# Kernel tuning notes

Hardware: AMD Instinct MI355X
Metric: run time of the kernel (lower is better)

Reference implementation:

```python
import jax, jax.numpy as jnp
import numpy as np

B, T, D = 2, 1024, 1024
H, HKV = 16, 8
HD = D // H           # 64
NREP = H // HKV       # 2
NLAYERS = 3
MAXKV = T * NLAYERS   # 3072
EPS = 1e-5


def setup_inputs() -> dict:
    key = jax.random.key(0)
    ks = jax.random.split(key, 8)
    # rotary tables over full accumulated-KV range
    inv_freq = 1.0 / (10000.0 ** (jnp.arange(0, HD, 2, dtype=jnp.float32) / HD))  # (HD/2,)
    t = jnp.arange(MAXKV, dtype=jnp.float32)
    freqs = jnp.outer(t, inv_freq)  # (MAXKV, HD/2)
    return {
        "x": jax.random.normal(ks[0], (B, T, D), jnp.float32),
        "cos": jnp.cos(freqs),
        "sin": jnp.sin(freqs),
        "q_w": jax.random.normal(ks[1], (NLAYERS, D, D), jnp.float32) * 0.02,
        "k_w": jax.random.normal(ks[2], (NLAYERS, D // NREP, D), jnp.float32) * 0.02,
        "v_w": jax.random.normal(ks[3], (NLAYERS, D // NREP, D), jnp.float32) * 0.02,
        "ln_w": jnp.ones((NLAYERS, D), jnp.float32),
        "lam": jax.random.normal(ks[4], (NLAYERS,), jnp.float32) * 0.1,
        "out_w": jax.random.normal(ks[5], (D, D), jnp.float32) * 0.02,
        "final_ln_w": jnp.ones((D,), jnp.float32),
        "alpha": jnp.ones((1,), jnp.float32),
    }


def rmsnorm(x, w):
    return x * jax.lax.rsqrt(jnp.mean(x * x, axis=-1, keepdims=True) + EPS) * w


def rope(x, cos, sin):
    # x: (B, L, h, HD); cos/sin: (MAXKV, HD/2); flash_attn non-interleaved rotary
    L = x.shape[1]
    c = jnp.concatenate([cos[:L], cos[:L]], axis=-1)[None, :, None, :]
    s = jnp.concatenate([sin[:L], sin[:L]], axis=-1)[None, :, None, :]
    x1, x2 = jnp.split(x, 2, axis=-1)
    rot = jnp.concatenate([-x2, x1], axis=-1)
    return x * c + rot * s


def reference(x, cos, sin, q_w, k_w, v_w, ln_w, lam, out_w, final_ln_w, alpha):
    scale = HD ** -0.5
    # lambda weights: layernorm over sigmoid of the 3 scalars (biased var, eps=1e-5)
    s = jax.nn.sigmoid(lam)
    lw = (s - s.mean()) * jax.lax.rsqrt(s.var() + EPS)
    qidx = jnp.arange(T)
    k_list, v_list = [], []
    acc = jnp.zeros_like(x)
    for i in range(NLAYERS):
        q = (x @ q_w[i].T).reshape(B, T, H, HD)
        k = (x @ k_w[i].T).reshape(B, T, HKV, HD)
        v = (x @ v_w[i].T).reshape(B, T, HKV, HD)
        k_list.append(k)
        v_list.append(v)
        K = jnp.concatenate(k_list, axis=1)  # (B, L, HKV, HD), L=(i+1)*T
        V = jnp.concatenate(v_list, axis=1)
        L = K.shape[1]
        qr = rope(q, cos, sin)
        Kr = rope(K, cos, sin)  # whole buffer re-rotated each layer, as in original
        Kr = jnp.repeat(Kr, NREP, axis=2)  # GQA expand
        Vr = jnp.repeat(V, NREP, axis=2)
        scores = jnp.einsum('bqhd,bkhd->bhqk', qr, Kr) * scale
        # flash_attn causal=True with kv_len > q_len aligns bottom-right
        mask = jnp.arange(L)[None, :] <= (qidx + (L - T))[:, None]
        scores = jnp.where(mask[None, None], scores, -jnp.inf)
        attn = jax.nn.softmax(scores, axis=-1)
        o = jnp.einsum('bhqk,bkhd->bqhd', attn, Vr).reshape(B, T, D)
        acc = acc + rmsnorm(o, ln_w[i]) * lw[i]
    out = rmsnorm(acc + alpha * x, final_ln_w)
    return out @ out_w.T
```

## Files before the change

### kernel.cpp

```cpp
#include <hip/hip_runtime.h>
#include <type_traits>
#include <utility>

typedef unsigned short u16;
typedef unsigned int u32;
typedef short short8 __attribute__((ext_vector_type(8)));
typedef __bf16 bf16x8 __attribute__((ext_vector_type(8)));
typedef float floatx4 __attribute__((ext_vector_type(4)));

template <typename V, typename = void> struct MfmaTakes : std::false_type {};
template <typename V>
struct MfmaTakes<V, std::void_t<decltype(__builtin_amdgcn_mfma_f32_16x16x32_bf16(
    std::declval<V>(), std::declval<V>(), std::declval<floatx4>(), 0, 0, 0))>>
    : std::true_type {};

template <typename V>
__device__ __forceinline__ floatx4 mfma_impl(V a, V b, floatx4 c, std::true_type) {
  return __builtin_amdgcn_mfma_f32_16x16x32_bf16(a, b, c, 0, 0, 0);
}
template <typename V>
__device__ __forceinline__ floatx4 mfma_impl(V a, V b, floatx4 c, std::false_type) {
  return __builtin_amdgcn_mfma_f32_16x16x32_bf16(
      __builtin_bit_cast(bf16x8, a), __builtin_bit_cast(bf16x8, b), c, 0, 0, 0);
}
__device__ __forceinline__ floatx4 MFMA16(short8 a, short8 b, floatx4 c) {
  return mfma_impl<short8>(a, b, c, MfmaTakes<short8>{});
}

__device__ __forceinline__ u16 f2bf(float f) {
  union { float f; unsigned u; } x; x.f = f;
  unsigned r = (x.u + 0x7fffu + ((x.u >> 16) & 1u)) >> 16;
  return (u16)r;
}
__device__ __forceinline__ float bf2f(u16 v) {
  union { unsigned u; float f; } x; x.u = ((unsigned)v) << 16; return x.f;
}
__device__ __forceinline__ u32 packbf(float lo, float hi) {
  return (__float_as_uint(hi) & 0xffff0000u) | (__float_as_uint(lo) >> 16);
}

#if defined(__has_builtin)
#if __has_builtin(__builtin_amdgcn_global_load_lds)
#define HAS_GLLDS 1
#endif
#endif
__device__ __forceinline__ void stage16(const u16* g, u16* lbase, int lane) {
#ifdef HAS_GLLDS
  __builtin_amdgcn_global_load_lds(
      (__attribute__((address_space(1))) void*)(g),
      (__attribute__((address_space(3))) void*)(lbase), 16, 0, 0);
#else
  *(uint4*)(lbase + lane * 8) = *(const uint4*)g;
#endif
}

__global__ __launch_bounds__(256) void prep_kernel(
    const float* __restrict__ x, const float* __restrict__ qw,
    const float* __restrict__ kw, const float* __restrict__ vw,
    const float* __restrict__ outw, const float* __restrict__ lam,
    u16* __restrict__ xb, u16* __restrict__ wcat, u16* __restrict__ outwb,
    float* __restrict__ lwbuf) {
  size_t gid = (size_t)blockIdx.x * 256 + threadIdx.x;
  if (gid == 0) {
    float s0 = 1.f / (1.f + expf(-lam[0]));
    float s1 = 1.f / (1.f + expf(-lam[1]));
    float s2 = 1.f / (1.f + expf(-lam[2]));
    float mean = (s0 + s1 + s2) * (1.f / 3.f);
    float d0 = s0 - mean, d1 = s1 - mean, d2 = s2 - mean;
    float var = (d0 * d0 + d1 * d1 + d2 * d2) * (1.f / 3.f);
    float r = rsqrtf(var + 1e-5f);
    lwbuf[0] = d0 * r; lwbuf[1] = d1 * r; lwbuf[2] = d2 * r;
  }
  if (gid < 524288) {
    float4 v = ((const float4*)x)[gid];
    ushort4 o; o.x = f2bf(v.x); o.y = f2bf(v.y); o.z = f2bf(v.z); o.w = f2bf(v.w);
    ((ushort4*)xb)[gid] = o;
    return;
  }
  size_t g2 = gid - 524288;
  if (g2 < 1572864) {
    int col4 = (int)(g2 & 255);
    int n = (int)(g2 >> 8);
    int layer = n >> 11, r = n & 2047;
    const float* srcrow;
    if (r < 1024) srcrow = qw + ((size_t)(layer * 1024 + r) << 10);
    else if (r < 1536) srcrow = kw + ((size_t)(layer * 512 + (r - 1024)) << 10);
    else srcrow = vw + ((size_t)(layer * 512 + (r - 1536)) << 10);
    float4 v = ((const float4*)srcrow)[col4];
    ushort4 o; o.x = f2bf(v.x); o.y = f2bf(v.y); o.z = f2bf(v.z); o.w = f2bf(v.w);
    ((ushort4*)wcat)[g2] = o;
    return;
  }
  size_t g3 = g2 - 1572864;
  if (g3 < 262144) {
    float4 v = ((const float4*)outw)[g3];
    ushort4 o; o.x = f2bf(v.x); o.y = f2bf(v.y); o.z = f2bf(v.z); o.w = f2bf(v.w);
    ((ushort4*)outwb)[g3] = o;
  }
}

__global__ __launch_bounds__(256) void gemm128(
    const u16* __restrict__ A, const u16* __restrict__ Bw,
    void* __restrict__ Cp, int N, int K, int obf16) {
  __shared__ u16 As[128][64];
  __shared__ u16 Bs[128][64];
  const unsigned flat = blockIdx.x;
  const int bm = (flat >> 3) & 15;
  const int bn = ((flat >> 7) << 3) + (flat & 7);
  const int tid = threadIdx.x;
  const int wave = tid >> 6, lane = tid & 63;
  const int quad = lane >> 4, l16 = lane & 15;
  const int wm = wave & 1, wn = wave >> 1;
  const int srow = lane >> 3, skc = (lane & 7) * 8;
  floatx4 acc[4][4];
#pragma unroll
  for (int i = 0; i < 4; i++)
#pragma unroll
    for (int j = 0; j < 4; j++) { acc[i][j][0] = 0.f; acc[i][j][1] = 0.f; acc[i][j][2] = 0.f; acc[i][j][3] = 0.f; }
  const u16* Abase = A + (size_t)(bm * 128) * K;
  const u16* Bbase = Bw + (size_t)(bn * 128) * K;
  for (int k0 = 0; k0 < K; k0 += 64) {
    __syncthreads();
#pragma unroll
    for (int i = 0; i < 4; i++) {
      int ch = wave * 4 + i;
      stage16(Abase + (size_t)(ch * 8 + srow) * K + k0 + skc, &As[ch * 8][0], lane);
      stage16(Bbase + (size_t)(ch * 8 + srow) * K + k0 + skc, &Bs[ch * 8][0], lane);
    }
    __syncthreads();
#pragma unroll
    for (int kf = 0; kf < 2; kf++) {
      short8 af[4], bf[4];
#pragma unroll
      for (int mi = 0; mi < 4; mi++)
        af[mi] = *(const short8*)(&As[wm * 64 + mi * 16 + l16][kf * 32 + quad * 8]);
#pragma unroll
      for (int ni = 0; ni < 4; ni++)
        bf[ni] = *(const short8*)(&Bs[wn * 64 + ni * 16 + l16][kf * 32 + quad * 8]);
#pragma unroll
      for (int mi = 0; mi < 4; mi++)
#pragma unroll
        for (int ni = 0; ni < 4; ni++)
          acc[mi][ni] = MFMA16(af[mi], bf[ni], acc[mi][ni]);
    }
  }
  float* Cf = (float*)Cp;
  u16* Cb = (u16*)Cp;
#pragma unroll
  for (int mi = 0; mi < 4; mi++)
#pragma unroll
    for (int ni = 0; ni < 4; ni++)
#pragma unroll
      for (int r = 0; r < 4; r++) {
        int row = bm * 128 + wm * 64 + mi * 16 + quad * 4 + r;
        int col = bn * 128 + wn * 64 + ni * 16 + l16;
        if (obf16) Cb[(size_t)row * N + col] = f2bf(acc[mi][ni][r]);
        else Cf[(size_t)row * N + col] = acc[mi][ni][r];
      }
}

__global__ __launch_bounds__(256) void gemm_bt(
    const u16* __restrict__ A, const u16* __restrict__ Bw,
    float* __restrict__ C, int N, int K) {
  __shared__ u16 As[64][72];
  __shared__ u16 Bs[64][72];
  const int bm = blockIdx.x, bn = blockIdx.y;
  const int tid = threadIdx.x;
  const int wave = tid >> 6, lane = tid & 63;
  const int quad = lane >> 4, l16 = lane & 15;
  const int lr = tid >> 2, lc = (tid & 3) << 4;
  floatx4 acc[4];
#pragma unroll
  for (int i = 0; i < 4; i++) { acc[i][0] = 0.f; acc[i][1] = 0.f; acc[i][2] = 0.f; acc[i][3] = 0.f; }
  const u16* Arow = A + (size_t)(bm * 64 + lr) * K;
  const u16* Brow = Bw + (size_t)(bn * 64 + lr) * K;
  for (int k0 = 0; k0 < K; k0 += 64) {
    __syncthreads();
    *(uint4*)(&As[lr][lc])     = *(const uint4*)(Arow + k0 + lc);
    *(uint4*)(&As[lr][lc + 8]) = *(const uint4*)(Arow + k0 + lc + 8);
    *(uint4*)(&Bs[lr][lc])     = *(const uint4*)(Brow + k0 + lc);
    *(uint4*)(&Bs[lr][lc + 8]) = *(const uint4*)(Brow + k0 + lc + 8);
    __syncthreads();
    const int mrow = wave * 16 + l16;
    short8 a0 = *(const short8*)(&As[mrow][quad * 8]);
    short8 a1 = *(const short8*)(&As[mrow][32 + quad * 8]);
#pragma unroll
    for (int ns = 0; ns < 4; ns++) {
      short8 b0 = *(const short8*)(&Bs[ns * 16 + l16][quad * 8]);
      short8 b1 = *(const short8*)(&Bs[ns * 16 + l16][32 + quad * 8]);
      acc[ns] = MFMA16(a0, b0, acc[ns]);
      acc[ns] = MFMA16(a1, b1, acc[ns]);
    }
  }
#pragma unroll
  for (int ns = 0; ns < 4; ns++)
#pragma unroll
    for (int r = 0; r < 4; r++) {
      int row = bm * 64 + wave * 16 + quad * 4 + r;
      int col = bn * 64 + ns * 16 + l16;
      C[(size_t)row * N + col] = acc[ns][r];
    }
}

__global__ __launch_bounds__(256) void reshape_kernel(
    const u16* __restrict__ qkvb, const float* __restrict__ cosb,
    const float* __restrict__ sinb, u16* __restrict__ qr,
    u16* __restrict__ kr, u16* __restrict__ vtg) {
  __shared__ u16 T[64][72];
  const int bid = blockIdx.x, tid = threadIdx.x;
  union U8 { uint4 v; u16 s[8]; };
  union F8 { float4 v[2]; float f[8]; };
  if (bid < 2304) {
    unsigned gid = (unsigned)bid * 256 + tid;
    if (gid < 393216u) {
      int d8 = gid & 3, t = (gid >> 2) & 1023, h = (gid >> 12) & 15;
      int b = (gid >> 16) & 1, layer = gid >> 17;
      size_t src = (size_t)(b * 1024 + t) * 6144 + layer * 2048 + h * 64 + d8 * 8;
      U8 xa, xc; xa.v = *(const uint4*)(qkvb + src); xc.v = *(const uint4*)(qkvb + src + 32);
      F8 C, S;
      const float4* cp = (const float4*)(cosb + (size_t)t * 32 + d8 * 8);
      const float4* sp = (const float4*)(sinb + (size_t)t * 32 + d8 * 8);
      C.v[0] = cp[0]; C.v[1] = cp[1]; S.v[0] = sp[0]; S.v[1] = sp[1];
      U8 o1, o2;
#pragma unroll
      for (int j = 0; j < 8; j++) {
        float x1 = bf2f(xa.s[j]), x2 = bf2f(xc.s[j]);
        o1.s[j] = f2bf((x1 * C.f[j] - x2 * S.f[j]) * 0.125f);
        o2.s[j] = f2bf((x2 * C.f[j] + x1 * S.f[j]) * 0.125f);
      }
      size_t dst = ((((size_t)layer * 2 + b) * 16 + h) * 1024 + t) * 64 + d8 * 8;
      *(uint4*)(qr + dst) = o1.v;
      *(uint4*)(qr + dst + 32) = o2.v;
      return;
    }
    unsigned g2 = gid - 393216u;
    if (g2 < 196608u) {
      int d8 = g2 & 3, t = (g2 >> 2) & 1023, h = (g2 >> 12) & 7;
      int b = (g2 >> 15) & 1, layer = g2 >> 16;
      int pos = layer * 1024 + t;
      size_t src = (size_t)(b * 1024 + t) * 6144 + layer * 2048 + 1024 + h * 64 + d8 * 8;
      U8 xa, xc; xa.v = *(const uint4*)(qkvb + src); xc.v = *(const uint4*)(qkvb + src + 32);
      F8 C, S;
      const float4* cp = (const float4*)(cosb + (size_t)pos * 32 + d8 * 8);
      const float4* sp = (const float4*)(sinb + (size_t)pos * 32 + d8 * 8);
      C.v[0] = cp[0]; C.v[1] = cp[1]; S.v[0] = sp[0]; S.v[1] = sp[1];
      U8 o1, o2;
#pragma unroll
      for (int j = 0; j < 8; j++) {
        float x1 = bf2f(xa.s[j]), x2 = bf2f(xc.s[j]);
        o1.s[j] = f2bf(x1 * C.f[j] - x2 * S.f[j]);
        o2.s[j] = f2bf(x2 * C.f[j] + x1 * S.f[j]);
      }
      size_t dst = (((size_t)b * 8 + h) * 3072 + pos) * 64 + d8 * 8;
      *(uint4*)(kr + dst) = o1.v;
      *(uint4*)(kr + dst + 32) = o2.v;
    }
    return;
  }
  const int b2 = bid - 2304;
  const int xt = b2 & 15;
  const int y = b2 >> 4;
  const int layer = y >> 4, b = (y >> 3) & 1, h = y & 7;
  const int t0 = xt * 64;
  {
    const int p = tid >> 2, dc = (tid & 3) * 16;
    const u16* src = qkvb + (size_t)(b * 1024 + t0 + p) * 6144 + layer * 2048 + 1536 + h * 64 + dc;
    U8 u0, u1;
    u0.v = *(const uint4*)(src);
    u1.v = *(const uint4*)(src + 8);
#pragma unroll
    for (int j = 0; j < 8; j++) { T[dc + j][p] = u0.s[j]; T[dc + 8 + j][p] = u1.s[j]; }
  }
  __syncthreads();
  {
    const int d = tid >> 2, pc = (tid & 3) * 16;
    u16* dst = vtg + ((size_t)((b * 8 + h) * 64 + d)) * 3072 + layer * 1024 + t0 + pc;
    *(uint4*)(dst) = *(const uint4*)(&T[d][pc]);
    *(uint4*)(dst + 8) = *(const uint4*)(&T[d][pc + 8]);
  }
}

__global__ __launch_bounds__(256) void attn_v5(
    const u16* __restrict__ qr, const u16* __restrict__ kr,
    const u16* __restrict__ vt, float* __restrict__ obS,
    float* __restrict__ lbufp) {
  __shared__ u16 Kt[32][72];
  __shared__ u16 Vtt[64][40];
  __shared__ u16 Pw[4][16][40];
  const unsigned flat = blockIdx.x;
  const int bhz = (int)((flat >> 6) * 8 + (flat & 7));
  const int qtile = 7 - (int)((flat >> 3) & 7);
  const int z = bhz >> 5;
  const int bh = bhz & 31;
  const int lay = (z == 5) ? 0 : ((z == 0 || z == 4) ? 1 : 2);
  const int n = lay * 32 + qtile * 4 + 4;
  int kt0, kt1;
  if (lay == 0) { kt0 = 0; kt1 = n; }
  else if (lay == 1) { int hf = n >> 1; kt0 = (z == 0) ? 0 : hf; kt1 = (z == 0) ? hf : n; }
  else {
    int t1 = n / 3, t2 = (2 * n) / 3;
    kt0 = (z == 1) ? 0 : ((z == 2) ? t1 : t2);
    kt1 = (z == 1) ? t1 : ((z == 2) ? t2 : n);
  }
  const int maskkt = lay * 32 + qtile * 4;
  const int b = bh >> 4, h = bh & 15, hk = h >> 1;
  const int tid = threadIdx.x, wave = tid >> 6, lane = tid & 63;
  const int quad = lane >> 4, l16 = lane & 15;
  const int qeffbase = lay * 1024 + qtile * 128 + wave * 32;
  const u16* qpb = qr + ((((size_t)lay * 2 + b) * 16 + h) * 1024
                         + qtile * 128 + wave * 32 + l16) * 64 + quad * 8;
  short8 qf[2][2];
  qf[0][0] = *(const short8*)(qpb);
  qf[0][1] = *(const short8*)(qpb + 32);
  qf[1][0] = *(const short8*)(qpb + 1024);
  qf[1][1] = *(const short8*)(qpb + 1056);
  const short8 ones = {16256, 16256, 16256, 16256, 16256, 16256, 16256, 16256};
  floatx4 oacc[2][4];
#pragma unroll
  for (int nt = 0; nt < 2; nt++)
#pragma unroll
    for (int dt = 0; dt < 4; dt++) { oacc[nt][dt][0] = 0.f; oacc[nt][dt][1] = 0.f; oacc[nt][dt][2] = 0.f; oacc[nt][dt][3] = 0.f; }
  floatx4 lacc[2];
  lacc[0][0] = 0.f; lacc[0][1] = 0.f; lacc[0][2] = 0.f; lacc[0][3] = 0.f;
  lacc[1] = lacc[0];
  const int ksr = tid >> 3, ksc = (tid & 7) * 8;
  const int vdr = tid >> 2, vdc = (tid & 3) * 8;
  const u16* kp = kr + ((size_t)(b * 8 + hk) * 3072 + kt0 * 32 + ksr) * 64 + ksc;
  const u16* vp = vt + ((size_t)(b * 8 + hk) * 64 + vdr) * 3072 + kt0 * 32 + vdc;
  uint4 kA = *(const uint4*)kp;
  uint4 vA = *(const uint4*)vp;
  for (int kt = kt0; kt < kt1; kt++) {
    kp += 2048; vp += 32;
    __syncthreads();
    *(uint4*)(&Kt[ksr][ksc])  = kA;
    *(uint4*)(&Vtt[vdr][vdc]) = vA;
    if (kt + 1 < kt1) { kA = *(const uint4*)kp; vA = *(const uint4*)vp; }
    __syncthreads();
    const bool needmask = (kt >= maskkt);
    uint2 pk[2][2];
#pragma unroll
    for (int mt = 0; mt < 2; mt++) {
      short8 kfa = *(const short8*)(&Kt[mt * 16 + l16][quad * 8]);
      short8 kfb = *(const short8*)(&Kt[mt * 16 + l16][32 + quad * 8]);
      const int keyb = kt * 32 + mt * 16 + quad * 4;
#pragma unroll
      for (int nt = 0; nt < 2; nt++) {
        floatx4 s; s[0] = 0.f; s[1] = 0.f; s[2] = 0.f; s[3] = 0.f;
        s = MFMA16(kfa, qf[nt][0], s);
        s = MFMA16(kfb, qf[nt][1], s);
        float p0 = __expf(s[0]), p1 = __expf(s[1]);
        float p2 = __expf(s[2]), p3 = __expf(s[3]);
        if (needmask) {
          int qpos = qeffbase + nt * 16 + l16;
          if (keyb + 0 > qpos) p0 = 0.f;
          if (keyb + 1 > qpos) p1 = 0.f;
          if (keyb + 2 > qpos) p2 = 0.f;
          if (keyb + 3 > qpos) p3 = 0.f;
        }
        pk[mt][nt].x = packbf(p0, p1);
        pk[mt][nt].y = packbf(p2, p3);
      }
    }
    short8 vf[4];
#pragma unroll
    for (int dt = 0; dt < 4; dt++)
      vf[dt] = *(const short8*)(&Vtt[dt * 16 + l16][quad * 8]);
#pragma unroll
    for (int nt = 0; nt < 2; nt++) {
      *(uint2*)(&Pw[wave][l16][quad * 4])      = pk[0][nt];
      *(uint2*)(&Pw[wave][l16][16 + quad * 4]) = pk[1][nt];
      short8 pf = *(const short8*)(&Pw[wave][l16][quad * 8]);
      lacc[nt] = MFMA16(ones, pf, lacc[nt]);
#pragma unroll
      for (int dt = 0; dt < 4; dt++)
        oacc[nt][dt] = MFMA16(vf[dt], pf, oacc[nt][dt]);
    }
  }
  float* Pf = (float*)(&Pw[wave][0][0]);
  const int tt = lane >> 2, dd = (lane & 3) << 2;
#pragma unroll
  for (int nt = 0; nt < 2; nt++) {
    int t = qtile * 128 + wave * 32 + nt * 16 + l16;
    if (quad == 0)
      lbufp[((size_t)z * 2048 + b * 1024 + t) * 16 + h] = lacc[nt][0];
    int t2 = qtile * 128 + wave * 32 + nt * 16 + tt;
    float* orow = obS + ((size_t)(z * 2 + b) * 1024 + t2) * 1024 + h * 64 + dd;
#pragma unroll
    for (int dt = 0; dt < 4; dt++) {
      *(floatx4*)(&Pf[l16 * 20 + quad * 4]) = oacc[nt][dt];
      floatx4 val = *(const floatx4*)(&Pf[tt * 20 + dd]);
      *(floatx4*)(orow + dt * 16) = val;
    }
  }
}

__device__ __forceinline__ float block_sum(float v, float* red) {
  v += __shfl_xor(v, 32); v += __shfl_xor(v, 16); v += __shfl_xor(v, 8);
  v += __shfl_xor(v, 4);  v += __shfl_xor(v, 2);  v += __shfl_xor(v, 1);
  __syncthreads();
  if ((threadIdx.x & 63) == 0) red[threadIdx.x >> 6] = v;
  __syncthreads();
  return red[0] + red[1] + red[2] + red[3];
}

__global__ __launch_bounds__(256) void fused_norm(
    const float* __restrict__ obS, const float* __restrict__ lbufp,
    const float* __restrict__ x, const float* __restrict__ lnw,
    const float* __restrict__ lwbuf, const float* __restrict__ flnw,
    const float* __restrict__ alphap, u16* __restrict__ y) {
  __shared__ float red[4];
  const int row = blockIdx.x, tid = threadIdx.x;
  float a[4] = {0.f, 0.f, 0.f, 0.f};
  const int nsl[3] = {1, 2, 3};
  const int sl[3][3] = {{5, 0, 0}, {0, 4, 0}, {1, 2, 3}};
#pragma unroll
  for (int l = 0; l < 3; l++) {
    float o0 = 0.f, o1 = 0.f, o2 = 0.f, o3 = 0.f, ls = 0.f;
#pragma unroll
    for (int si = 0; si < 3; si++) {
      if (si >= nsl[l]) break;
      int z = sl[l][si];
      float4 v = ((const float4*)(obS + ((size_t)z * 2048 + row) * 1024))[tid];
      o0 += v.x; o1 += v.y; o2 += v.z; o3 += v.w;
      ls += lbufp[((size_t)z * 2048 + row) * 16 + (tid >> 4)];
    }
    float linv = 1.f / ls;
    float v0 = o0 * linv, v1 = o1 * linv, v2 = o2 * linv, v3 = o3 * linv;
    float ss = v0 * v0 + v1 * v1 + v2 * v2 + v3 * v3;
    ss = block_sum(ss, red);
    float rstd = rsqrtf(ss * (1.f / 1024.f) + 1e-5f);
    float lw = lwbuf[l];
    float4 w = ((const float4*)(lnw + (size_t)l * 1024))[tid];
    a[0] += v0 * rstd * w.x * lw;
    a[1] += v1 * rstd * w.y * lw;
    a[2] += v2 * rstd * w.z * lw;
    a[3] += v3 * rstd * w.w * lw;
  }
  const float aa = alphap[0];
  float4 xv = ((const float4*)(x + (size_t)row * 1024))[tid];
  float v0 = a[0] + aa * xv.x, v1 = a[1] + aa * xv.y;
  float v2 = a[2] + aa * xv.z, v3 = a[3] + aa * xv.w;
  float ss = v0 * v0 + v1 * v1 + v2 * v2 + v3 * v3;
  ss = block_sum(ss, red);
  float rstd = rsqrtf(ss * (1.f / 1024.f) + 1e-5f);
  float4 fw = ((const float4*)flnw)[tid];
  ushort4 o;
  o.x = f2bf(v0 * rstd * fw.x); o.y = f2bf(v1 * rstd * fw.y);
  o.z = f2bf(v2 * rstd * fw.z); o.w = f2bf(v3 * rstd * fw.w);
  ((ushort4*)(y + (size_t)row * 1024))[tid] = o;
}

extern "C" void kernel_launch(void* const* d_in, const int* in_sizes, int n_in,
                              void* d_out, int out_size, void* d_ws, size_t ws_size,
                              hipStream_t stream) {
  const float* x     = (const float*)d_in[0];
  const float* cosb  = (const float*)d_in[1];
  const float* sinb  = (const float*)d_in[2];
  const float* qw    = (const float*)d_in[3];
  const float* kw    = (const float*)d_in[4];
  const float* vw    = (const float*)d_in[5];
  const float* lnw   = (const float*)d_in[6];
  const float* lam   = (const float*)d_in[7];
  const float* outw  = (const float*)d_in[8];
  const float* flnw  = (const float*)d_in[9];
  const float* alphap= (const float*)d_in[10];
  float* out = (float*)d_out;
  char* ws = (char*)d_ws;
  u16*   xb    = (u16*)  (ws + 0);
  u16*   wcat  = (u16*)  (ws + 4194304);
  u16*   qkvb  = (u16*)  (ws + 16777216);
  float* obS   = (float*)(ws + 0);
  u16*   outwb = (u16*)  (ws + 50331648);
  float* lwbuf = (float*)(ws + 52428800);
  u16*   qr    = (u16*)  (ws + 52429824);
  u16*   kr    = (u16*)  (ws + 65012736);
  u16*   vt    = (u16*)  (ws + 71304192);
  float* lbufp = (float*)(ws + 77595648);
  u16*   yb    = (u16*)  (ws + 78382080);

  prep_kernel<<<9216, 256, 0, stream>>>(x, qw, kw, vw, outw, lam, xb, wcat, outwb, lwbuf);
  gemm128<<<768, 256, 0, stream>>>(xb, wcat, qkvb, 6144, 1024, 1);
  reshape_kernel<<<3072, 256, 0, stream>>>(qkvb, cosb, sinb, qr, kr, vt);
  attn_v5<<<1536, 256, 0, stream>>>(qr, kr, vt, obS, lbufp);
  fused_norm<<<2048, 256, 0, stream>>>(obS, lbufp, x, lnw, lwbuf, flnw, alphap, yb);
  gemm_bt<<<dim3(32, 16), 256, 0, stream>>>(yb, outwb, out, 1024, 1024);
}
```

Before: 262.5 us.

## Fuse RoPE and QKV reshape into GEMM epilogue; store attention partials in bf16

The QKV GEMM epilogue now applies rotary embedding, the attention scale, and the head-major/transposed-V layout directly, which removes the separate reshape kernel and the bf16 qkv intermediate round trip. Attention split partial outputs are also written as bf16 instead of fp32, halving that traffic into the norm kernel. In exchange the epilogue stores are narrower and scattered: 2-byte Q/K writes and strided V writes. The partials also lose precision before summation.

```diff
diff --git a/kernel.cpp b/kernel.cpp
--- a/kernel.cpp
+++ b/kernel.cpp
@@ -37,6 +37,9 @@
 }
 __device__ __forceinline__ u32 packbf(float lo, float hi) {
   return (__float_as_uint(hi) & 0xffff0000u) | (__float_as_uint(lo) >> 16);
+}
+__device__ __forceinline__ u32 pack2bf(float lo, float hi) {
+  return ((u32)f2bf(hi) << 16) | (u32)f2bf(lo);
 }
 
 #if defined(__has_builtin)
@@ -99,9 +102,10 @@
   }
 }
 
-__global__ __launch_bounds__(256) void gemm128(
+__global__ __launch_bounds__(256) void gemm_qkv(
     const u16* __restrict__ A, const u16* __restrict__ Bw,
-    void* __restrict__ Cp, int N, int K, int obf16) {
+    const float* __restrict__ cosb, const float* __restrict__ sinb,
+    u16* __restrict__ qr, u16* __restrict__ kr, u16* __restrict__ vt) {
   __shared__ u16 As[128][64];
   __shared__ u16 Bs[128][64];
   const unsigned flat = blockIdx.x;
@@ -117,15 +121,15 @@
   for (int i = 0; i < 4; i++)
 #pragma unroll
     for (int j = 0; j < 4; j++) { acc[i][j][0] = 0.f; acc[i][j][1] = 0.f; acc[i][j][2] = 0.f; acc[i][j][3] = 0.f; }
-  const u16* Abase = A + (size_t)(bm * 128) * K;
-  const u16* Bbase = Bw + (size_t)(bn * 128) * K;
-  for (int k0 = 0; k0 < K; k0 += 64) {
+  const u16* Abase = A + (size_t)(bm * 128) * 1024;
+  const u16* Bbase = Bw + (size_t)(bn * 128) * 1024;
+  for (int k0 = 0; k0 < 1024; k0 += 64) {
     __syncthreads();
 #pragma unroll
     for (int i = 0; i < 4; i++) {
       int ch = wave * 4 + i;
-      stage16(Abase + (size_t)(ch * 8 + srow) * K + k0 + skc, &As[ch * 8][0], lane);
-      stage16(Bbase + (size_t)(ch * 8 + srow) * K + k0 + skc, &Bs[ch * 8][0], lane);
+      stage16(Abase + (size_t)(ch * 8 + srow) * 1024 + k0 + skc, &As[ch * 8][0], lane);
+      stage16(Bbase + (size_t)(ch * 8 + srow) * 1024 + k0 + skc, &Bs[ch * 8][0], lane);
     }
     __syncthreads();
 #pragma unroll
@@ -144,19 +148,69 @@
           acc[mi][ni] = MFMA16(af[mi], bf[ni], acc[mi][ni]);
     }
   }
-  float* Cf = (float*)Cp;
-  u16* Cb = (u16*)Cp;
-#pragma unroll
-  for (int mi = 0; mi < 4; mi++)
-#pragma unroll
-    for (int ni = 0; ni < 4; ni++)
-#pragma unroll
-      for (int r = 0; r < 4; r++) {
-        int row = bm * 128 + wm * 64 + mi * 16 + quad * 4 + r;
-        int col = bn * 128 + wn * 64 + ni * 16 + l16;
-        if (obf16) Cb[(size_t)row * N + col] = f2bf(acc[mi][ni][r]);
-        else Cf[(size_t)row * N + col] = acc[mi][ni][r];
+  const int f0 = bn * 128 + wn * 64;
+  const int lay = f0 >> 11;
+  const int r0 = f0 & 2047;
+  const int mrow0 = bm * 128 + wm * 64;
+  if (r0 < 1024) {
+    const int h = r0 >> 6;
+#pragma unroll
+    for (int mi = 0; mi < 4; mi++)
+#pragma unroll
+      for (int rr = 0; rr < 4; rr++) {
+        int m = mrow0 + mi * 16 + quad * 4 + rr;
+        int b = m >> 10, t = m & 1023;
+        const float* cp = cosb + (size_t)t * 32;
+        const float* sp = sinb + (size_t)t * 32;
+        float c0 = cp[l16], s0 = sp[l16];
+        float c1 = cp[16 + l16], s1 = sp[16 + l16];
+        float x10 = acc[mi][0][rr], x20 = acc[mi][2][rr];
+        float x11 = acc[mi][1][rr], x21 = acc[mi][3][rr];
+        u16* row = qr + ((((size_t)lay * 2 + b) * 16 + h) * 1024 + t) * 64;
+        row[l16]      = f2bf((x10 * c0 - x20 * s0) * 0.125f);
+        row[16 + l16] = f2bf((x11 * c1 - x21 * s1) * 0.125f);
+        row[32 + l16] = f2bf((x20 * c0 + x10 * s0) * 0.125f);
+        row[48 + l16] = f2bf((x21 * c1 + x11 * s1) * 0.125f);
       }
+  } else if (r0 < 1536) {
+    const int hk = (r0 - 1024) >> 6;
+#pragma unroll
+    for (int mi = 0; mi < 4; mi++)
+#pragma unroll
+      for (int rr = 0; rr < 4; rr++) {
+        int m = mrow0 + mi * 16 + quad * 4 + rr;
+        int b = m >> 10, t = m & 1023;
+        int pos = lay * 1024 + t;
+        const float* cp = cosb + (size_t)pos * 32;
+        const float* sp = sinb + (size_t)pos * 32;
+        float c0 = cp[l16], s0 = sp[l16];
+        float c1 = cp[16 + l16], s1 = sp[16 + l16];
+        float x10 = acc[mi][0][rr], x20 = acc[mi][2][rr];
+        float x11 = acc[mi][1][rr], x21 = acc[mi][3][rr];
+        u16* row = kr + (((size_t)(b * 8 + hk)) * 3072 + pos) * 64;
+        row[l16]      = f2bf(x10 * c0 - x20 * s0);
+        row[16 + l16] = f2bf(x11 * c1 - x21 * s1);
+        row[32 + l16] = f2bf(x20 * c0 + x10 * s0);
+        row[48 + l16] = f2bf(x21 * c1 + x11 * s1);
+      }
+  } else {
+    const int hv = (r0 - 1536) >> 6;
+#pragma unroll
+    for (int mi = 0; mi < 4; mi++) {
+      int m0 = mrow0 + mi * 16 + quad * 4;
+      int b = m0 >> 10;
+      int pos0 = lay * 1024 + (m0 & 1023);
+      u16* colbase = vt + ((size_t)(b * 8 + hv) * 64) * 3072 + pos0;
+#pragma unroll
+      for (int ni = 0; ni < 4; ni++) {
+        int d = ni * 16 + l16;
+        uint2 st;
+        st.x = pack2bf(acc[mi][ni][0], acc[mi][ni][1]);
+        st.y = pack2bf(acc[mi][ni][2], acc[mi][ni][3]);
+        *(uint2*)(colbase + (size_t)d * 3072) = st;
+      }
+    }
+  }
 }
 
 __global__ __launch_bounds__(256) void gemm_bt(
@@ -202,87 +256,9 @@
     }
 }
 
-__global__ __launch_bounds__(256) void reshape_kernel(
-    const u16* __restrict__ qkvb, const float* __restrict__ cosb,
-    const float* __restrict__ sinb, u16* __restrict__ qr,
-    u16* __restrict__ kr, u16* __restrict__ vtg) {
-  __shared__ u16 T[64][72];
-  const int bid = blockIdx.x, tid = threadIdx.x;
-  union U8 { uint4 v; u16 s[8]; };
-  union F8 { float4 v[2]; float f[8]; };
-  if (bid < 2304) {
-    unsigned gid = (unsigned)bid * 256 + tid;
-    if (gid < 393216u) {
-      int d8 = gid & 3, t = (gid >> 2) & 1023, h = (gid >> 12) & 15;
-      int b = (gid >> 16) & 1, layer = gid >> 17;
-      size_t src = (size_t)(b * 1024 + t) * 6144 + layer * 2048 + h * 64 + d8 * 8;
-      U8 xa, xc; xa.v = *(const uint4*)(qkvb + src); xc.v = *(const uint4*)(qkvb + src + 32);
-      F8 C, S;
-      const float4* cp = (const float4*)(cosb + (size_t)t * 32 + d8 * 8);
-      const float4* sp = (const float4*)(sinb + (size_t)t * 32 + d8 * 8);
-      C.v[0] = cp[0]; C.v[1] = cp[1]; S.v[0] = sp[0]; S.v[1] = sp[1];
-      U8 o1, o2;
-#pragma unroll
-      for (int j = 0; j < 8; j++) {
-        float x1 = bf2f(xa.s[j]), x2 = bf2f(xc.s[j]);
-        o1.s[j] = f2bf((x1 * C.f[j] - x2 * S.f[j]) * 0.125f);
-        o2.s[j] = f2bf((x2 * C.f[j] + x1 * S.f[j]) * 0.125f);
-      }
-      size_t dst = ((((size_t)layer * 2 + b) * 16 + h) * 1024 + t) * 64 + d8 * 8;
-      *(uint4*)(qr + dst) = o1.v;
-      *(uint4*)(qr + dst + 32) = o2.v;
-      return;
-    }
-    unsigned g2 = gid - 393216u;
-    if (g2 < 196608u) {
-      int d8 = g2 & 3, t = (g2 >> 2) & 1023, h = (g2 >> 12) & 7;
-      int b = (g2 >> 15) & 1, layer = g2 >> 16;
-      int pos = layer * 1024 + t;
-      size_t src = (size_t)(b * 1024 + t) * 6144 + layer * 2048 + 1024 + h * 64 + d8 * 8;
-      U8 xa, xc; xa.v = *(const uint4*)(qkvb + src); xc.v = *(const uint4*)(qkvb + src + 32);
-      F8 C, S;
-      const float4* cp = (const float4*)(cosb + (size_t)pos * 32 + d8 * 8);
-      const float4* sp = (const float4*)(sinb + (size_t)pos * 32 + d8 * 8);
-      C.v[0] = cp[0]; C.v[1] = cp[1]; S.v[0] = sp[0]; S.v[1] = sp[1];
-      U8 o1, o2;
-#pragma unroll
-      for (int j = 0; j < 8; j++) {
-        float x1 = bf2f(xa.s[j]), x2 = bf2f(xc.s[j]);
-        o1.s[j] = f2bf(x1 * C.f[j] - x2 * S.f[j]);
-        o2.s[j] = f2bf(x2 * C.f[j] + x1 * S.f[j]);
-      }
-      size_t dst = (((size_t)b * 8 + h) * 3072 + pos) * 64 + d8 * 8;
-      *(uint4*)(kr + dst) = o1.v;
-      *(uint4*)(kr + dst + 32) = o2.v;
-    }
-    return;
-  }
-  const int b2 = bid - 2304;
-  const int xt = b2 & 15;
-  const int y = b2 >> 4;
-  const int layer = y >> 4, b = (y >> 3) & 1, h = y & 7;
-  const int t0 = xt * 64;
-  {
-    const int p = tid >> 2, dc = (tid & 3) * 16;
-    const u16* src = qkvb + (size_t)(b * 1024 + t0 + p) * 6144 + layer * 2048 + 1536 + h * 64 + dc;
-    U8 u0, u1;
-    u0.v = *(const uint4*)(src);
-    u1.v = *(const uint4*)(src + 8);
-#pragma unroll
-    for (int j = 0; j < 8; j++) { T[dc + j][p] = u0.s[j]; T[dc + 8 + j][p] = u1.s[j]; }
-  }
-  __syncthreads();
-  {
-    const int d = tid >> 2, pc = (tid & 3) * 16;
-    u16* dst = vtg + ((size_t)((b * 8 + h) * 64 + d)) * 3072 + layer * 1024 + t0 + pc;
-    *(uint4*)(dst) = *(const uint4*)(&T[d][pc]);
-    *(uint4*)(dst + 8) = *(const uint4*)(&T[d][pc + 8]);
-  }
-}
-
 __global__ __launch_bounds__(256) void attn_v5(
     const u16* __restrict__ qr, const u16* __restrict__ kr,
-    const u16* __restrict__ vt, float* __restrict__ obS,
+    const u16* __restrict__ vt, u16* __restrict__ obS,
     float* __restrict__ lbufp) {
   __shared__ u16 Kt[32][72];
   __shared__ u16 Vtt[64][40];
@@ -384,12 +360,13 @@
     if (quad == 0)
       lbufp[((size_t)z * 2048 + b * 1024 + t) * 16 + h] = lacc[nt][0];
     int t2 = qtile * 128 + wave * 32 + nt * 16 + tt;
-    float* orow = obS + ((size_t)(z * 2 + b) * 1024 + t2) * 1024 + h * 64 + dd;
+    u16* orow = obS + ((size_t)(z * 2 + b) * 1024 + t2) * 1024 + h * 64 + dd;
 #pragma unroll
     for (int dt = 0; dt < 4; dt++) {
       *(floatx4*)(&Pf[l16 * 20 + quad * 4]) = oacc[nt][dt];
       floatx4 val = *(const floatx4*)(&Pf[tt * 20 + dd]);
-      *(floatx4*)(orow + dt * 16) = val;
+      uint2 st; st.x = pack2bf(val[0], val[1]); st.y = pack2bf(val[2], val[3]);
+      *(uint2*)(orow + dt * 16) = st;
     }
   }
 }
@@ -404,7 +381,7 @@
 }
 
 __global__ __launch_bounds__(256) void fused_norm(
-    const float* __restrict__ obS, const float* __restrict__ lbufp,
+    const u16* __restrict__ obS, const float* __restrict__ lbufp,
     const float* __restrict__ x, const float* __restrict__ lnw,
     const float* __restrict__ lwbuf, const float* __restrict__ flnw,
     const float* __restrict__ alphap, u16* __restrict__ y) {
@@ -420,8 +397,9 @@
     for (int si = 0; si < 3; si++) {
       if (si >= nsl[l]) break;
       int z = sl[l][si];
-      float4 v = ((const float4*)(obS + ((size_t)z * 2048 + row) * 1024))[tid];
-      o0 += v.x; o1 += v.y; o2 += v.z; o3 += v.w;
+      uint2 v = ((const uint2*)(obS + ((size_t)z * 2048 + row) * 1024))[tid];
+      o0 += bf2f((u16)(v.x & 0xffff)); o1 += bf2f((u16)(v.x >> 16));
+      o2 += bf2f((u16)(v.y & 0xffff)); o3 += bf2f((u16)(v.y >> 16));
       ls += lbufp[((size_t)z * 2048 + row) * 16 + (tid >> 4)];
     }
     float linv = 1.f / ls;
@@ -468,19 +446,17 @@
   char* ws = (char*)d_ws;
   u16*   xb    = (u16*)  (ws + 0);
   u16*   wcat  = (u16*)  (ws + 4194304);
-  u16*   qkvb  = (u16*)  (ws + 16777216);
-  float* obS   = (float*)(ws + 0);
-  u16*   outwb = (u16*)  (ws + 50331648);
-  float* lwbuf = (float*)(ws + 52428800);
-  u16*   qr    = (u16*)  (ws + 52429824);
-  u16*   kr    = (u16*)  (ws + 65012736);
-  u16*   vt    = (u16*)  (ws + 71304192);
-  float* lbufp = (float*)(ws + 77595648);
-  u16*   yb    = (u16*)  (ws + 78382080);
+  u16*   obS   = (u16*)  (ws + 0);
+  u16*   outwb = (u16*)  (ws + 25165824);
+  float* lwbuf = (float*)(ws + 27262976);
+  u16*   qr    = (u16*)  (ws + 27264000);
+  u16*   kr    = (u16*)  (ws + 39846912);
+  u16*   vt    = (u16*)  (ws + 46138368);
+  float* lbufp = (float*)(ws + 52429824);
+  u16*   yb    = (u16*)  (ws + 53216256);
 
   prep_kernel<<<9216, 256, 0, stream>>>(x, qw, kw, vw, outw, lam, xb, wcat, outwb, lwbuf);
-  gemm128<<<768, 256, 0, stream>>>(xb, wcat, qkvb, 6144, 1024, 1);
-  reshape_kernel<<<3072, 256, 0, stream>>>(qkvb, cosb, sinb, qr, kr, vt);
+  gemm_qkv<<<768, 256, 0, stream>>>(xb, wcat, cosb, sinb, qr, kr, vt);
   attn_v5<<<1536, 256, 0, stream>>>(qr, kr, vt, obS, lbufp);
   fused_norm<<<2048, 256, 0, stream>>>(obS, lbufp, x, lnw, lwbuf, flnw, alphap, yb);
   gemm_bt<<<dim3(32, 16), 256, 0, stream>>>(yb, outwb, out, 1024, 1024);
```

Result: faster. 252.0 us (-4.0%).
